# Performance work log

Measured on AMD Instinct MI355X. Metric: run time of the kernel, lower is better.

The kernel has to match this reference:

```python
import jax, jax.numpy as jnp
import numpy as np

FP8_E4M3_MAX = 448.0  # max representable magnitude in float8_e4m3fn


def setup_inputs() -> dict:
    key = jax.random.key(0)
    k1, k2, k3 = jax.random.split(key, 3)
    n_tokens, d_in, d_out = 8192, 4096, 16384
    x = jax.random.normal(k1, (n_tokens, d_in), dtype=jnp.float32)
    # weight stored in fp8 domain (values stand in for dequantized-by-scale fp8 codes)
    weight = jax.random.normal(k2, (d_out, d_in), dtype=jnp.float32)
    bias = jax.random.normal(k3, (d_out,), dtype=jnp.float32) * 0.1
    input_scale = jnp.float32(0.05)   # per-tensor activation scale
    weight_scale = jnp.float32(0.01)  # per-tensor weight scale
    return {"x": x, "weight": weight, "bias": bias,
            "input_scale": input_scale, "weight_scale": weight_scale}


def reference(x, weight, bias, input_scale, weight_scale):
    # fp8 qdq path: quantize activation to fp8 e4m3 domain (fake-quant: scale + clamp),
    # then scaled GEMM: out = (x_q @ W_q^T) * (input_scale * weight_scale) + bias,
    # matching cublas_scaled_mm(input, weight.t(), scale_a, scale_b) + bias.
    x_q = jnp.clip(x / input_scale, -FP8_E4M3_MAX, FP8_E4M3_MAX)  # [T, d_in]
    acc = jnp.einsum('ti,oi->to', x_q, weight)                     # [T, d_out]
    out = acc * (input_scale * weight_scale) + bias
    return out
```

## Files before the change

### kernel.cpp

```cpp
#include <hip/hip_runtime.h>
#include <stdint.h>
#include <stddef.h>


typedef _Float16 half8 __attribute__((ext_vector_type(8)));
typedef _Float16 half4v __attribute__((ext_vector_type(4)));
typedef float f32x4 __attribute__((ext_vector_type(4)));

#define BM 256
#define BN 256
#define BK 64
#define FP8MAX 448.0f

__device__ __forceinline__ void gload_lds16(const _Float16* g, _Float16* lds) {
  __builtin_amdgcn_global_load_lds(
      (const __attribute__((address_space(1))) uint32_t*)g,
      (__attribute__((address_space(3))) uint32_t*)lds, 16, 0, 0);
}

#define BAR() asm volatile("s_barrier" ::: "memory")
#define WAIT_VM(N) asm volatile("s_waitcnt vmcnt(" #N ")" ::: "memory")
#define LGKM0() asm volatile("s_waitcnt lgkmcnt(0)" ::: "memory")
#define SCHED_FENCE() __builtin_amdgcn_sched_barrier(0)

#define MFMA_Q(AF, BF, MG, NG) do {                                           \
  __builtin_amdgcn_s_setprio(1);                                              \
  _Pragma("unroll")                                                           \
  for (int mf_ = 0; mf_ < 4; ++mf_) {                                         \
    _Pragma("unroll")                                                         \
    for (int nf_ = 0; nf_ < 2; ++nf_) {                                       \
      _Pragma("unroll")                                                       \
      for (int ks_ = 0; ks_ < 2; ++ks_)                                       \
        acc[(MG)*4 + mf_][(NG)*2 + nf_] =                                     \
            __builtin_amdgcn_mfma_f32_16x16x32_f16(                           \
                AF[mf_*2 + ks_], BF[nf_*2 + ks_],                             \
                acc[(MG)*4 + mf_][(NG)*2 + nf_], 0, 0, 0);                    \
    }                                                                         \
  }                                                                           \
  __builtin_amdgcn_s_setprio(0);                                              \
} while (0)

__global__ void cvt_x_kernel(const float* __restrict__ x, _Float16* __restrict__ xq,
                             const float* __restrict__ s_ptr, long n4) {
  float inv = 1.0f / s_ptr[0];
  long i = (long)blockIdx.x * blockDim.x + threadIdx.x;
  long stride = (long)gridDim.x * blockDim.x;
  const float4* x4 = (const float4*)x;
  for (long j = i; j < n4; j += stride) {
    float4 v = x4[j];
    half4v h;
    h[0] = (_Float16)fminf(fmaxf(v.x * inv, -FP8MAX), FP8MAX);
    h[1] = (_Float16)fminf(fmaxf(v.y * inv, -FP8MAX), FP8MAX);
    h[2] = (_Float16)fminf(fmaxf(v.z * inv, -FP8MAX), FP8MAX);
    h[3] = (_Float16)fminf(fmaxf(v.w * inv, -FP8MAX), FP8MAX);
    *(half4v*)(xq + j * 4) = h;
  }
}

__global__ void cvt_w_kernel(const float* __restrict__ w, _Float16* __restrict__ wq,
                             long n4) {
  long i = (long)blockIdx.x * blockDim.x + threadIdx.x;
  long stride = (long)gridDim.x * blockDim.x;
  const float4* w4 = (const float4*)w;
  for (long j = i; j < n4; j += stride) {
    float4 v = w4[j];
    half4v h;
    h[0] = (_Float16)v.x; h[1] = (_Float16)v.y;
    h[2] = (_Float16)v.z; h[3] = (_Float16)v.w;
    *(half4v*)(wq + j * 4) = h;
  }
}

__global__ __launch_bounds__(512, 2)
void gemm256_sw(const _Float16* __restrict__ A, const _Float16* __restrict__ B,
                const float* __restrict__ bias, const float* __restrict__ is_ptr,
                const float* __restrict__ ws_ptr, float* __restrict__ out,
                int M, int N, int K) {
  __shared__ __align__(16) _Float16 sA[2][256 * 64];
  __shared__ __align__(16) _Float16 sB[2][256 * 64];

  const int nbn = N / BN;
  const int nwg = gridDim.x;
  int wg = blockIdx.x;
  if ((nwg & 7) == 0) {
    int q = nwg >> 3;
    wg = (wg & 7) * q + (wg >> 3);
  }
  const int brow = (wg / nbn) * BM;
  const int bcol = (wg % nbn) * BN;

  const int tid  = threadIdx.x;
  const int lane = tid & 63;
  const int w    = tid >> 6;
  const int wr   = w >> 2;
  const int wc   = w & 3;

  const size_t lsrc = (size_t)(lane >> 3) * K + (size_t)((lane & 7) ^ (lane >> 3)) * 8;
  const _Float16* gA = A + (size_t)brow * K + lsrc;
  const _Float16* gB = B + (size_t)bcol * K + lsrc;

  auto stageA = [&](int buf, int pi, int kt) {
    gload_lds16(gA + (size_t)(pi * 64 + w * 8) * K + kt,
                &sA[buf][(pi * 512 + w * 64) * 8]);
  };
  auto stageB = [&](int buf, int pi, int kt) {
    gload_lds16(gB + (size_t)(pi * 64 + w * 8) * K + kt,
                &sB[buf][(pi * 512 + w * 64) * 8]);
  };

  const int rdbase = (lane & 15) * 64;
  const int e0 = rdbase + (((lane >> 4) + 0) ^ (lane & 7)) * 8;
  const int e1 = rdbase + (((lane >> 4) + 4) ^ (lane & 7)) * 8;

  auto ldA = [&](int buf, int mg, half8* a) {
#pragma unroll
    for (int mf = 0; mf < 4; ++mf) {
      const int base = (wr * 8 + mg * 4 + mf) * 1024;
      a[mf * 2 + 0] = *(const half8*)&sA[buf][base + e0];
      a[mf * 2 + 1] = *(const half8*)&sA[buf][base + e1];
    }
  };
  auto ldB = [&](int buf, int ng, half8* b) {
#pragma unroll
    for (int nf = 0; nf < 2; ++nf) {
      const int base = (wc * 4 + ng * 2 + nf) * 1024;
      b[nf * 2 + 0] = *(const half8*)&sB[buf][base + e0];
      b[nf * 2 + 1] = *(const half8*)&sB[buf][base + e1];
    }
  };

  f32x4 acc[8][4] = {};
  const int NT = K / BK;

  stageA(0, 0, 0); stageA(0, 1, 0); stageA(0, 2, 0); stageA(0, 3, 0);
  stageB(0, 0, 0); stageB(0, 1, 0); stageB(0, 2, 0); stageB(0, 3, 0);
  stageA(1, 0, BK); stageA(1, 1, BK); stageA(1, 2, BK); stageA(1, 3, BK);
  WAIT_VM(4);
  BAR();

  for (int t = 0; t < NT; ++t) {
    const int cur = t & 1, nxt = cur ^ 1;
    const int ktB = (t + 1) * BK;
    const int ktA = (t + 2) * BK;
    const bool sb = (t + 1) < NT;
    const bool sa = (t + 2) < NT;
    half8 aL[8], aH[8], bL[4], bH[4];

    ldA(cur, 0, aL); ldB(cur, 0, bL);
    if (sb) { stageB(nxt, 0, ktB); stageB(nxt, 1, ktB); }
    BAR();
    LGKM0(); SCHED_FENCE();
    MFMA_Q(aL, bL, 0, 0);
    BAR();

    ldA(cur, 1, aH);
    if (sb) { stageB(nxt, 2, ktB); stageB(nxt, 3, ktB); }
    BAR();
    LGKM0(); SCHED_FENCE();
    MFMA_Q(aH, bL, 1, 0);
    BAR();

    ldB(cur, 1, bH);
    if (sa) { stageA(cur, 0, ktA); stageA(cur, 1, ktA); }
    BAR();
    LGKM0(); SCHED_FENCE();
    MFMA_Q(aH, bH, 1, 1);
    BAR();

    if (sa) { stageA(cur, 2, ktA); stageA(cur, 3, ktA); }
    MFMA_Q(aL, bH, 0, 1);
    if (t < NT - 2)       WAIT_VM(4);
    else if (t == NT - 2) WAIT_VM(0);
    BAR();
  }

  const float sc = is_ptr[0] * ws_ptr[0];
  const int orow = brow + wr * 128;
  const int ocol = bcol + wc * 64;
#pragma unroll
  for (int n = 0; n < 4; ++n) {
    const int col = ocol + n * 16 + (lane & 15);
    const float bv = bias[col];
#pragma unroll
    for (int m = 0; m < 8; ++m) {
#pragma unroll
      for (int r = 0; r < 4; ++r) {
        const int row = orow + m * 16 + (lane >> 4) * 4 + r;
        out[(size_t)row * N + col] = acc[m][n][r] * sc + bv;
      }
    }
  }
}

extern "C" void kernel_launch(void* const* d_in, const int* in_sizes, int n_in,
                              void* d_out, int out_size, void* d_ws, size_t ws_size,
                              hipStream_t stream) {
  const float* x    = (const float*)d_in[0];
  const float* wgt  = (const float*)d_in[1];
  const float* bias = (const float*)d_in[2];
  const float* is   = (const float*)d_in[3];
  const float* wsc  = (const float*)d_in[4];
  float* out = (float*)d_out;

  const long x_n = in_sizes[0];
  const long w_n = in_sizes[1];
  const int  N   = in_sizes[2];
  const int  K   = (int)(w_n / N);
  const int  M   = (int)(x_n / K);

  _Float16* xq = (_Float16*)d_ws;
  _Float16* wq = xq + x_n;

  cvt_x_kernel<<<2048, 256, 0, stream>>>(x, xq, is, x_n >> 2);
  cvt_w_kernel<<<2048, 256, 0, stream>>>(wgt, wq, w_n >> 2);

  const int nwg = (M / BM) * (N / BN);
  gemm256_sw<<<nwg, 512, 0, stream>>>(xq, wq, bias, is, wsc, out, M, N, K);
}
```

Before: 1.270 ms.

## Restructure GEMM main loop into two phases with partial LDS waits

The main loop drops from four barrier-separated quarter phases to two. All LDS fragment reads for the tile are issued up front, and partial lgkmcnt waits let the first MFMA quarters start while the remaining reads are still in flight. B staging for the next tile is grouped into one batch, followed by a single barrier, then all A staging and the remaining MFMAs. This removes several barriers per iteration, at the cost of keeping all A and B fragments live at once, which raises register pressure. It also depends on correct lgkmcnt counting, since mixing LDS reads with global-to-LDS loads could make the partial waits inexact.

```diff
diff --git a/kernel.cpp b/kernel.cpp
--- a/kernel.cpp
+++ b/kernel.cpp
@@ -20,7 +20,7 @@
 
 #define BAR() asm volatile("s_barrier" ::: "memory")
 #define WAIT_VM(N) asm volatile("s_waitcnt vmcnt(" #N ")" ::: "memory")
-#define LGKM0() asm volatile("s_waitcnt lgkmcnt(0)" ::: "memory")
+#define WAIT_LGKM(N) asm volatile("s_waitcnt lgkmcnt(" #N ")" ::: "memory")
 #define SCHED_FENCE() __builtin_amdgcn_sched_barrier(0)
 
 #define MFMA_Q(AF, BF, MG, NG) do {                                           \
@@ -72,7 +72,7 @@
 }
 
 __global__ __launch_bounds__(512, 2)
-void gemm256_sw(const _Float16* __restrict__ A, const _Float16* __restrict__ B,
+void gemm256_p2(const _Float16* __restrict__ A, const _Float16* __restrict__ B,
                 const float* __restrict__ bias, const float* __restrict__ is_ptr,
                 const float* __restrict__ ws_ptr, float* __restrict__ out,
                 int M, int N, int K) {
@@ -147,30 +147,27 @@
     half8 aL[8], aH[8], bL[4], bH[4];
 
     ldA(cur, 0, aL); ldB(cur, 0, bL);
-    if (sb) { stageB(nxt, 0, ktB); stageB(nxt, 1, ktB); }
+    SCHED_FENCE();
+    ldB(cur, 1, bH);
+    SCHED_FENCE();
+    ldA(cur, 1, aH);
+    SCHED_FENCE();
+    if (sb) { stageB(nxt, 0, ktB); stageB(nxt, 1, ktB);
+              stageB(nxt, 2, ktB); stageB(nxt, 3, ktB); }
+
+    WAIT_LGKM(12); SCHED_FENCE();
+    MFMA_Q(aL, bL, 0, 0);
+    WAIT_LGKM(8); SCHED_FENCE();
+    MFMA_Q(aL, bH, 0, 1);
+    WAIT_LGKM(0); SCHED_FENCE();
     BAR();
-    LGKM0(); SCHED_FENCE();
-    MFMA_Q(aL, bL, 0, 0);
-    BAR();
-
-    ldA(cur, 1, aH);
-    if (sb) { stageB(nxt, 2, ktB); stageB(nxt, 3, ktB); }
-    BAR();
-    LGKM0(); SCHED_FENCE();
+
+    if (sa) { stageA(cur, 0, ktA); stageA(cur, 1, ktA);
+              stageA(cur, 2, ktA); stageA(cur, 3, ktA); }
+    MFMA_Q(aH, bH, 1, 1);
     MFMA_Q(aH, bL, 1, 0);
-    BAR();
-
-    ldB(cur, 1, bH);
-    if (sa) { stageA(cur, 0, ktA); stageA(cur, 1, ktA); }
-    BAR();
-    LGKM0(); SCHED_FENCE();
-    MFMA_Q(aH, bH, 1, 1);
-    BAR();
-
-    if (sa) { stageA(cur, 2, ktA); stageA(cur, 3, ktA); }
-    MFMA_Q(aL, bH, 0, 1);
-    if (t < NT - 2)       WAIT_VM(4);
-    else if (t == NT - 2) WAIT_VM(0);
+
+    if (t < NT - 2) { WAIT_VM(4); } else { WAIT_VM(0); }
     BAR();
   }
 
@@ -215,5 +212,5 @@
   cvt_w_kernel<<<2048, 256, 0, stream>>>(wgt, wq, w_n >> 2);
 
   const int nwg = (M / BM) * (N / BN);
-  gemm256_sw<<<nwg, 512, 0, stream>>>(xq, wq, bias, is, wsc, out, M, N, K);
-}
+  gemm256_p2<<<nwg, 512, 0, stream>>>(xq, wq, bias, is, wsc, out, M, N, K);
+}
```

Measured after the change: 1.192 ms. -6.1%, faster.
